# Kernel tuning notes

Hardware: AMD Instinct MI355X
Metric: run time of the kernel (lower is better)

## Reference

```python
import jax, jax.numpy as jnp
import numpy as np

B, IN, OUT = 64, 1024, 1024

def setup_inputs() -> dict:
    key = jax.random.key(0)
    ks = jax.random.split(key, 7)
    return {
        "x": jax.random.normal(ks[0], (B, IN), dtype=jnp.float32),
        "mu": jax.random.normal(ks[1], (IN, OUT), dtype=jnp.float32),
        "ro": jax.random.normal(ks[2], (IN, OUT), dtype=jnp.float32),
        "mu_bias": jax.random.normal(ks[3], (1, OUT), dtype=jnp.float32),
        "ro_bias": jax.random.normal(ks[4], (1, OUT), dtype=jnp.float32),
        "eps": jax.random.normal(ks[5], (B, IN, OUT), dtype=jnp.float32),
        "eps_bias": jax.random.normal(ks[6], (B, OUT), dtype=jnp.float32),
    }

def reference(x, mu, ro, mu_bias, ro_bias, eps, eps_bias):
    # sigma = log(1 + exp(ro))  (softplus), same for bias
    sigma = jax.nn.softplus(ro)            # [IN, OUT]
    sigma_bias = jax.nn.softplus(ro_bias)  # [1, OUT]
    weights = eps * sigma + mu             # [B, IN, OUT] per-sample weights
    bias = eps_bias * sigma_bias + mu_bias # [B, OUT]
    # batched matvec: x[b,i] @ weights[b,i,o] -> [B, OUT]
    out = jnp.einsum("bi,bio->bo", x, weights) + bias
    return out
```

## Files before the change

### kernel.cpp

```cpp
#include <hip/hip_runtime.h>


#define BB   64
#define INN  1024
#define OUTT 1024
#define B_T  4
#define ICH  32
#define I_C  (INN / ICH)

typedef float f4 __attribute__((ext_vector_type(4)));

__device__ __forceinline__ float softplus_f(float v) {
    return fmaxf(v, 0.0f) + log1pf(__expf(-fabsf(v)));
}

__global__ __launch_bounds__(256) void bayes_sig(
    const float* __restrict__ ro, float* __restrict__ sig)
{
    const int g = blockIdx.x * 256 + threadIdx.x;
    const f4 r = *(const f4*)(ro + (size_t)g * 4);
    f4 s;
    s.x = softplus_f(r.x); s.y = softplus_f(r.y);
    s.z = softplus_f(r.z); s.w = softplus_f(r.w);
    *(f4*)(sig + (size_t)g * 4) = s;
}

__global__ __launch_bounds__(256) void bayes_main(
    const float* __restrict__ x,
    const float* __restrict__ mu,
    const float* __restrict__ sig,
    const float* __restrict__ eps,
    float* __restrict__ part)
{
    __shared__ float xs[B_T][I_C];

    const int t  = threadIdx.x;
    const int o  = t << 2;
    const int c  = blockIdx.x;
    const int b0 = blockIdx.y * B_T;
    const int i0 = c * I_C;

    if (t < B_T * I_C) {
        const int b  = t / I_C;
        const int il = t % I_C;
        xs[b][il] = x[(b0 + b) * INN + i0 + il];
    }
    __syncthreads();

    f4 acc[B_T];
#pragma unroll
    for (int b = 0; b < B_T; ++b) acc[b] = (f4)0.0f;

#pragma unroll 4
    for (int il = 0; il < I_C; ++il) {
        const int i = i0 + il;
        const f4 sg4 = *(const f4*)(sig + (size_t)i * OUTT + o);
        const f4 mu4 = *(const f4*)(mu  + (size_t)i * OUTT + o);
#pragma unroll
        for (int b = 0; b < B_T; ++b) {
            const float xb = xs[b][il];
            const f4 e = __builtin_nontemporal_load(
                (const f4*)(eps + ((size_t)(b0 + b) * INN + i) * OUTT + o));
            acc[b].x = fmaf(xb, fmaf(e.x, sg4.x, mu4.x), acc[b].x);
            acc[b].y = fmaf(xb, fmaf(e.y, sg4.y, mu4.y), acc[b].y);
            acc[b].z = fmaf(xb, fmaf(e.z, sg4.z, mu4.z), acc[b].z);
            acc[b].w = fmaf(xb, fmaf(e.w, sg4.w, mu4.w), acc[b].w);
        }
    }

#pragma unroll
    for (int b = 0; b < B_T; ++b) {
        *(f4*)(part + ((size_t)(b0 + b) * ICH + c) * OUTT + o) = acc[b];
    }
}

__global__ __launch_bounds__(256) void bayes_reduce(
    const float* __restrict__ part,
    const float* __restrict__ mu_bias,
    const float* __restrict__ ro_bias,
    const float* __restrict__ eps_bias,
    float* __restrict__ out)
{
    const int g  = blockIdx.x * 256 + threadIdx.x;
    const int b  = g >> 8;
    const int o  = (g & 255) << 2;

    f4 s = (f4)0.0f;
#pragma unroll
    for (int c = 0; c < ICH; ++c) {
        const f4 p = *(const f4*)(part + ((size_t)b * ICH + c) * OUTT + o);
        s.x += p.x; s.y += p.y; s.z += p.z; s.w += p.w;
    }

    const f4 rb = *(const f4*)(ro_bias + o);
    const f4 mb = *(const f4*)(mu_bias + o);
    const f4 eb = *(const f4*)(eps_bias + (size_t)b * OUTT + o);
    s.x += fmaf(eb.x, softplus_f(rb.x), mb.x);
    s.y += fmaf(eb.y, softplus_f(rb.y), mb.y);
    s.z += fmaf(eb.z, softplus_f(rb.z), mb.z);
    s.w += fmaf(eb.w, softplus_f(rb.w), mb.w);

    *(f4*)(out + (size_t)g * 4) = s;
}

__global__ __launch_bounds__(256) void bayes_mono(
    const float* __restrict__ x, const float* __restrict__ mu,
    const float* __restrict__ ro, const float* __restrict__ mu_bias,
    const float* __restrict__ ro_bias, const float* __restrict__ eps,
    const float* __restrict__ eps_bias, float* __restrict__ out)
{
    const int t = threadIdx.x;
    const int o = t << 2;
    const int b = blockIdx.x;

    f4 acc = (f4)0.0f;
    for (int i = 0; i < INN; ++i) {
        const float xb = x[b * INN + i];
        const f4 r4 = *(const f4*)(ro + (size_t)i * OUTT + o);
        const f4 m4 = *(const f4*)(mu + (size_t)i * OUTT + o);
        const f4 e  = *(const f4*)(eps + ((size_t)b * INN + i) * OUTT + o);
        acc.x = fmaf(xb, fmaf(e.x, softplus_f(r4.x), m4.x), acc.x);
        acc.y = fmaf(xb, fmaf(e.y, softplus_f(r4.y), m4.y), acc.y);
        acc.z = fmaf(xb, fmaf(e.z, softplus_f(r4.z), m4.z), acc.z);
        acc.w = fmaf(xb, fmaf(e.w, softplus_f(r4.w), m4.w), acc.w);
    }
    const f4 rb = *(const f4*)(ro_bias + o);
    const f4 mb = *(const f4*)(mu_bias + o);
    const f4 eb = *(const f4*)(eps_bias + (size_t)b * OUTT + o);
    acc.x += fmaf(eb.x, softplus_f(rb.x), mb.x);
    acc.y += fmaf(eb.y, softplus_f(rb.y), mb.y);
    acc.z += fmaf(eb.z, softplus_f(rb.z), mb.z);
    acc.w += fmaf(eb.w, softplus_f(rb.w), mb.w);
    *(f4*)(out + (size_t)b * OUTT + o) = acc;
}

extern "C" void kernel_launch(void* const* d_in, const int* in_sizes, int n_in,
                              void* d_out, int out_size, void* d_ws, size_t ws_size,
                              hipStream_t stream) {
    const float* x        = (const float*)d_in[0];
    const float* mu       = (const float*)d_in[1];
    const float* ro       = (const float*)d_in[2];
    const float* mu_bias  = (const float*)d_in[3];
    const float* ro_bias  = (const float*)d_in[4];
    const float* eps      = (const float*)d_in[5];
    const float* eps_bias = (const float*)d_in[6];
    float* out = (float*)d_out;

    const size_t sig_elems  = (size_t)INN * OUTT;
    const size_t part_elems = (size_t)BB * ICH * OUTT;
    const size_t need = (sig_elems + part_elems) * sizeof(float);

    if (ws_size >= need) {
        float* sig  = (float*)d_ws;
        float* part = sig + sig_elems;

        bayes_sig<<<sig_elems / 1024, 256, 0, stream>>>(ro, sig);
        dim3 grid(ICH, BB / B_T);
        bayes_main<<<grid, 256, 0, stream>>>(x, mu, sig, eps, part);
        bayes_reduce<<<(BB * OUTT / 4) / 256, 256, 0, stream>>>(
            part, mu_bias, ro_bias, eps_bias, out);
    } else {
        bayes_mono<<<BB, 256, 0, stream>>>(x, mu, ro, mu_bias, ro_bias,
                                           eps, eps_bias, out);
    }
}
```

Measured before the change: 370.1 us.

## Fuse softplus into main kernel, halve batch tile, parallelize partial reduction

```diff
diff --git a/kernel.cpp b/kernel.cpp
--- a/kernel.cpp
+++ b/kernel.cpp
@@ -4,31 +4,20 @@
 #define BB   64
 #define INN  1024
 #define OUTT 1024
-#define B_T  4
+#define B_T  2
 #define ICH  32
 #define I_C  (INN / ICH)
 
 typedef float f4 __attribute__((ext_vector_type(4)));
 
 __device__ __forceinline__ float softplus_f(float v) {
-    return fmaxf(v, 0.0f) + log1pf(__expf(-fabsf(v)));
-}
-
-__global__ __launch_bounds__(256) void bayes_sig(
-    const float* __restrict__ ro, float* __restrict__ sig)
-{
-    const int g = blockIdx.x * 256 + threadIdx.x;
-    const f4 r = *(const f4*)(ro + (size_t)g * 4);
-    f4 s;
-    s.x = softplus_f(r.x); s.y = softplus_f(r.y);
-    s.z = softplus_f(r.z); s.w = softplus_f(r.w);
-    *(f4*)(sig + (size_t)g * 4) = s;
+    return fmaxf(v, 0.0f) + __logf(1.0f + __expf(-fabsf(v)));
 }
 
 __global__ __launch_bounds__(256) void bayes_main(
     const float* __restrict__ x,
     const float* __restrict__ mu,
-    const float* __restrict__ sig,
+    const float* __restrict__ ro,
     const float* __restrict__ eps,
     float* __restrict__ part)
 {
@@ -54,17 +43,19 @@
 #pragma unroll 4
     for (int il = 0; il < I_C; ++il) {
         const int i = i0 + il;
-        const f4 sg4 = *(const f4*)(sig + (size_t)i * OUTT + o);
-        const f4 mu4 = *(const f4*)(mu  + (size_t)i * OUTT + o);
+        const f4 r4 = *(const f4*)(ro + (size_t)i * OUTT + o);
+        const f4 m4 = *(const f4*)(mu + (size_t)i * OUTT + o);
+        f4 sg;
+        sg.x = softplus_f(r4.x); sg.y = softplus_f(r4.y);
+        sg.z = softplus_f(r4.z); sg.w = softplus_f(r4.w);
 #pragma unroll
         for (int b = 0; b < B_T; ++b) {
             const float xb = xs[b][il];
-            const f4 e = __builtin_nontemporal_load(
-                (const f4*)(eps + ((size_t)(b0 + b) * INN + i) * OUTT + o));
-            acc[b].x = fmaf(xb, fmaf(e.x, sg4.x, mu4.x), acc[b].x);
-            acc[b].y = fmaf(xb, fmaf(e.y, sg4.y, mu4.y), acc[b].y);
-            acc[b].z = fmaf(xb, fmaf(e.z, sg4.z, mu4.z), acc[b].z);
-            acc[b].w = fmaf(xb, fmaf(e.w, sg4.w, mu4.w), acc[b].w);
+            const f4 e = *(const f4*)(eps + ((size_t)(b0 + b) * INN + i) * OUTT + o);
+            acc[b].x = fmaf(xb, fmaf(e.x, sg.x, m4.x), acc[b].x);
+            acc[b].y = fmaf(xb, fmaf(e.y, sg.y, m4.y), acc[b].y);
+            acc[b].z = fmaf(xb, fmaf(e.z, sg.z, m4.z), acc[b].z);
+            acc[b].w = fmaf(xb, fmaf(e.w, sg.w, m4.w), acc[b].w);
         }
     }
 
@@ -81,26 +72,38 @@
     const float* __restrict__ eps_bias,
     float* __restrict__ out)
 {
-    const int g  = blockIdx.x * 256 + threadIdx.x;
-    const int b  = g >> 8;
-    const int o  = (g & 255) << 2;
+    const int t   = threadIdx.x;
+    const int g   = blockIdx.x * 64 + (t >> 2);
+    const int sub = t & 3;
+    const int b   = g >> 8;
+    const int o   = (g & 255) << 2;
 
     f4 s = (f4)0.0f;
+    const int c0 = sub * (ICH / 4);
 #pragma unroll
-    for (int c = 0; c < ICH; ++c) {
-        const f4 p = *(const f4*)(part + ((size_t)b * ICH + c) * OUTT + o);
+    for (int cc = 0; cc < ICH / 4; ++cc) {
+        const f4 p = *(const f4*)(part + ((size_t)b * ICH + c0 + cc) * OUTT + o);
         s.x += p.x; s.y += p.y; s.z += p.z; s.w += p.w;
     }
 
-    const f4 rb = *(const f4*)(ro_bias + o);
-    const f4 mb = *(const f4*)(mu_bias + o);
-    const f4 eb = *(const f4*)(eps_bias + (size_t)b * OUTT + o);
-    s.x += fmaf(eb.x, softplus_f(rb.x), mb.x);
-    s.y += fmaf(eb.y, softplus_f(rb.y), mb.y);
-    s.z += fmaf(eb.z, softplus_f(rb.z), mb.z);
-    s.w += fmaf(eb.w, softplus_f(rb.w), mb.w);
+#pragma unroll
+    for (int m = 1; m < 4; m <<= 1) {
+        s.x += __shfl_xor(s.x, m, 4);
+        s.y += __shfl_xor(s.y, m, 4);
+        s.z += __shfl_xor(s.z, m, 4);
+        s.w += __shfl_xor(s.w, m, 4);
+    }
 
-    *(f4*)(out + (size_t)g * 4) = s;
+    if (sub == 0) {
+        const f4 rb = *(const f4*)(ro_bias + o);
+        const f4 mb = *(const f4*)(mu_bias + o);
+        const f4 eb = *(const f4*)(eps_bias + (size_t)b * OUTT + o);
+        s.x += fmaf(eb.x, softplus_f(rb.x), mb.x);
+        s.y += fmaf(eb.y, softplus_f(rb.y), mb.y);
+        s.z += fmaf(eb.z, softplus_f(rb.z), mb.z);
+        s.w += fmaf(eb.w, softplus_f(rb.w), mb.w);
+        *(f4*)(out + (size_t)g * 4) = s;
+    }
 }
 
 __global__ __launch_bounds__(256) void bayes_mono(
@@ -146,18 +149,15 @@
     const float* eps_bias = (const float*)d_in[6];
     float* out = (float*)d_out;
 
-    const size_t sig_elems  = (size_t)INN * OUTT;
     const size_t part_elems = (size_t)BB * ICH * OUTT;
-    const size_t need = (sig_elems + part_elems) * sizeof(float);
+    const size_t need = part_elems * sizeof(float);
 
     if (ws_size >= need) {
-        float* sig  = (float*)d_ws;
-        float* part = sig + sig_elems;
+        float* part = (float*)d_ws;
 
-        bayes_sig<<<sig_elems / 1024, 256, 0, stream>>>(ro, sig);
         dim3 grid(ICH, BB / B_T);
-        bayes_main<<<grid, 256, 0, stream>>>(x, mu, sig, eps, part);
-        bayes_reduce<<<(BB * OUTT / 4) / 256, 256, 0, stream>>>(
+        bayes_main<<<grid, 256, 0, stream>>>(x, mu, ro, eps, part);
+        bayes_reduce<<<256, 256, 0, stream>>>(
             part, mu_bias, ro_bias, eps_bias, out);
     } else {
         bayes_mono<<<BB, 256, 0, stream>>>(x, mu, ro, mu_bias, ro_bias,
```

New measurement: 382.0 us. 3.2% more time.
